# Kernel optimization log

Hardware: AMD Instinct MI355X
Metric: run time of the kernel (lower is better)

The kernel has to match this reference:

```python
import jax, jax.numpy as jnp
import numpy as np

B, L, K, D = 1024, 8, 16, 64
_KSCALE = 1.0 / np.sqrt(K * D)  # keep channel roughly norm-preserving over layers


def setup_inputs() -> dict:
    key = jax.random.key(0)
    k1, k2, k3, k4 = jax.random.split(key, 4)
    state_re = jax.random.normal(k1, (B, D, D), dtype=jnp.float32)
    state_im = jax.random.normal(k2, (B, D, D), dtype=jnp.float32)
    kraus_re = jax.random.normal(k3, (L, K, D, D), dtype=jnp.float32) * _KSCALE
    kraus_im = jax.random.normal(k4, (L, K, D, D), dtype=jnp.float32) * _KSCALE
    return {"state_re": state_re, "state_im": state_im,
            "kraus_re": kraus_re, "kraus_im": kraus_im}


def reference(state_re, state_im, kraus_re, kraus_im):
    # rho: [B, d, d] complex density matrices; kraus: [L, K, d, d]
    rho = (state_re + 1j * state_im).astype(jnp.complex64)
    kraus = (kraus_re + 1j * kraus_im).astype(jnp.complex64)

    def layer_step(rho, Kl):
        # Kl: [K, d, d]. output_state = sum_k  K_k @ rho @ K_k^dagger
        tmp = jnp.einsum('kij,bjl->kbil', Kl, rho)            # K_k @ rho
        rho_new = jnp.einsum('kbil,kml->bim', tmp, Kl.conj())  # (...) @ K_k^dagger, summed over k
        return rho_new, None

    rho, _ = jax.lax.scan(layer_step, rho, kraus)
    # return real/imag stacked as float32: [2, B, d, d]
    return jnp.stack([rho.real, rho.imag])
```

## Files before the change

kernel.cpp:

```cpp
#include <hip/hip_runtime.h>
#include <hip/hip_fp16.h>

#define D 64
#define NKR 16
#define NB 1024
#define NL 8

typedef __attribute__((ext_vector_type(8))) _Float16 half8;
typedef __attribute__((ext_vector_type(16))) float f32x16;
typedef __attribute__((ext_vector_type(4))) int i32x4;

static __device__ __forceinline__ half8 neg8(half8 x) {
    i32x4 u = __builtin_bit_cast(i32x4, x);
    u = u ^ (int)0x80008000;
    return __builtin_bit_cast(half8, u);
}

static __device__ __forceinline__ unsigned pkrtz(float a, float b) {
    auto h = __builtin_amdgcn_cvt_pkrtz(a, b);
    return __builtin_bit_cast(unsigned, h);
}

static __device__ __forceinline__ void plswap(unsigned &a, unsigned &b) {
    asm volatile("v_permlane32_swap_b32 %0, %1" : "+v"(a), "+v"(b));
}

union Pack4 { _Float16 h[4]; uint2 u; };
union H8 { unsigned u[4]; uint2 v[2]; half8 h; };

#define MFMA __builtin_amdgcn_mfma_f32_32x32x16_f16


__global__ void kconv_kernel(const float* __restrict__ re, const float* __restrict__ im,
                             _Float16* __restrict__ out) {
    int plane = blockIdx.y;
    int idx = blockIdx.x * blockDim.x + threadIdx.x;
    const float* src = plane ? im : re;
    float4 v = ((const float4*)src)[idx];
    int e = idx * 4;
    int lk = e >> 12;
    int rem = e & 4095;
    int row = rem >> 6, col = rem & 63;
    int ihalf = row >> 5, r31 = row & 31;
    int ks = col >> 4, hl2 = (col >> 3) & 1, c = col & 7;
    Pack4 p;
    p.h[0] = (_Float16)v.x; p.h[1] = (_Float16)v.y;
    p.h[2] = (_Float16)v.z; p.h[3] = (_Float16)v.w;
    size_t off = (size_t)(lk * 2 + plane) * 4096 + ihalf * 2048
               + (2 * ks + hl2) * 256 + r31 * 8 + c;
    *(uint2*)(out + off) = p.u;
}

__global__ void sconv_kernel(const float* __restrict__ re, const float* __restrict__ im,
                             _Float16* __restrict__ out) {
    __shared__ float tile[64][65];
    int b = blockIdx.x;
    int t = threadIdx.x;
    for (int plane = 0; plane < 2; ++plane) {
        const float* src = (plane ? im : re) + (size_t)b * 4096;
        __syncthreads();
        #pragma unroll
        for (int i = 0; i < 16; ++i) {
            int e = t + 256 * i;
            tile[e >> 6][e & 63] = src[e];
        }
        __syncthreads();
        _Float16* o = out + ((size_t)b * 2 + plane) * 4096;
        #pragma unroll
        for (int i = 0; i < 16; ++i) {
            int oi = t + 256 * i;
            int lh = oi >> 11, slot = (oi >> 8) & 7, r = (oi >> 3) & 31, c = oi & 7;
            int col = 16 * (slot >> 1) + 8 * (slot & 1) + c;
            int row = 32 * lh + r;
            o[oi] = (_Float16)tile[col][row];
        }
    }
}

static __device__ __forceinline__ void exchange(const f32x16 &dd, half8 &f0, half8 &f1) {
    unsigned A0 = pkrtz(dd[0],  dd[1]),  B0 = pkrtz(dd[2],  dd[3]);
    unsigned A1 = pkrtz(dd[4],  dd[5]),  B1 = pkrtz(dd[6],  dd[7]);
    unsigned A2 = pkrtz(dd[8],  dd[9]),  B2 = pkrtz(dd[10], dd[11]);
    unsigned A3 = pkrtz(dd[12], dd[13]), B3 = pkrtz(dd[14], dd[15]);
    plswap(A0, A1);
    plswap(B0, B1);
    plswap(A2, A3);
    plswap(B2, B3);
    H8 h0; h0.u[0] = A0; h0.u[1] = B0; h0.u[2] = A1; h0.u[3] = B1; f0 = h0.h;
    H8 h1; h1.u[0] = A2; h1.u[1] = B2; h1.u[2] = A3; h1.u[3] = B3; f1 = h1.h;
}

template<int IT>
static __device__ __forceinline__ void kstep(
    const _Float16* __restrict__ kb,
    const half8 (&a1re)[2][4], const half8 (&a1im)[2][4],
    f32x16 (&accRe)[2], f32x16 (&accIm)[2],
    int lane)
{
    const _Float16* bo = kb + IT * 2048;
    const _Float16* bx = kb + (1 - IT) * 2048;

    half8 bre[4], bim[4];
    #pragma unroll
    for (int ks = 0; ks < 4; ++ks) {
        bre[ks] = *(const half8*)(bo + ks * 512 + lane * 8);
        bim[ks] = *(const half8*)(bo + 4096 + ks * 512 + lane * 8);
    }

    #pragma unroll
    for (int lh = 0; lh < 2; ++lh) {
        f32x16 ddre, ddim;
        #pragma unroll
        for (int i = 0; i < 16; ++i) { ddre[i] = 0.f; ddim[i] = 0.f; }
        __builtin_amdgcn_s_setprio(1);
        #pragma unroll
        for (int ks = 0; ks < 4; ++ks) {
            half8 bn = neg8(bim[ks]);
            ddre = MFMA(a1re[lh][ks], bre[ks], ddre, 0, 0, 0);
            ddre = MFMA(a1im[lh][ks], bn,      ddre, 0, 0, 0);
            ddim = MFMA(a1re[lh][ks], bim[ks], ddim, 0, 0, 0);
            ddim = MFMA(a1im[lh][ks], bre[ks], ddim, 0, 0, 0);
        }
        __builtin_amdgcn_s_setprio(0);

        half8 br2[2], bi2[2];
        #pragma unroll
        for (int c = 0; c < 2; ++c) {
            const int ks = 2 * lh + c;
            br2[c] = *(const half8*)(bx + ks * 512 + lane * 8);
            bi2[c] = *(const half8*)(bx + 4096 + ks * 512 + lane * 8);
        }

        half8 fre0, fre1, fim0, fim1;
        exchange(ddre, fre0, fre1);
        exchange(ddim, fim0, fim1);

        #pragma unroll
        for (int c = 0; c < 2; ++c) {
            const int ks = 2 * lh + c;
            half8 afre = c ? fre1 : fre0;
            half8 afim = c ? fim1 : fim0;
            half8 an  = neg8(afre);
            __builtin_amdgcn_s_setprio(1);
            accRe[IT]     = MFMA(afre, bre[ks], accRe[IT], 0, 0, 0);
            accRe[IT]     = MFMA(afim, bim[ks], accRe[IT], 0, 0, 0);
            accIm[IT]     = MFMA(afim, bre[ks], accIm[IT], 0, 0, 0);
            accIm[IT]     = MFMA(an,   bim[ks], accIm[IT], 0, 0, 0);
            accRe[1 - IT] = MFMA(afre, br2[c],  accRe[1 - IT], 0, 0, 0);
            accRe[1 - IT] = MFMA(afim, bi2[c],  accRe[1 - IT], 0, 0, 0);
            accIm[1 - IT] = MFMA(afim, br2[c],  accIm[1 - IT], 0, 0, 0);
            accIm[1 - IT] = MFMA(an,   bi2[c],  accIm[1 - IT], 0, 0, 0);
            __builtin_amdgcn_s_setprio(0);
        }
    }
}

template<int IT>
static __device__ __forceinline__ void run_layer(
    const _Float16* __restrict__ kraus,
    const half8 (&a1re)[2][4], const half8 (&a1im)[2][4],
    f32x16 (&accRe)[2], f32x16 (&accIm)[2],
    int lane)
{
    #pragma unroll 1
    for (int k = 0; k < NKR; ++k)
        kstep<IT>(kraus + (size_t)k * 8192, a1re, a1im, accRe, accIm, lane);
}

__global__ __launch_bounds__(64, 2) void layer_kernel(
    const _Float16* __restrict__ rho_in,
    _Float16* __restrict__ rho_out,
    float* __restrict__ final_out,
    const _Float16* __restrict__ kraus,
    int last)
{
    const int b    = blockIdx.x;
    const int IT   = blockIdx.y;
    const int lane = threadIdx.x;
    const int l31  = lane & 31;
    const int hl   = lane >> 5;

    half8 a1re[2][4], a1im[2][4];
    {
        const _Float16* rb = rho_in + (size_t)b * 2 * D * D;
        #pragma unroll
        for (int lh = 0; lh < 2; ++lh)
            #pragma unroll
            for (int ks = 0; ks < 4; ++ks) {
                a1re[lh][ks] = *(const half8*)(rb + lh * 2048 + ks * 512 + lane * 8);
                a1im[lh][ks] = *(const half8*)(rb + 4096 + lh * 2048 + ks * 512 + lane * 8);
            }
    }

    f32x16 accRe[2], accIm[2];
    #pragma unroll
    for (int mt = 0; mt < 2; ++mt)
        #pragma unroll
        for (int i = 0; i < 16; ++i) { accRe[mt][i] = 0.f; accIm[mt][i] = 0.f; }

    if (IT == 0) run_layer<0>(kraus, a1re, a1im, accRe, accIm, lane);
    else         run_layer<1>(kraus, a1re, a1im, accRe, accIm, lane);

    if (!last) {
        _Float16* ob = rho_out + (size_t)b * 2 * D * D;
        #pragma unroll
        for (int mt = 0; mt < 2; ++mt) {
            #pragma unroll
            for (int g = 0; g < 4; ++g) {
                Pack4 pr, pi;
                #pragma unroll
                for (int j = 0; j < 4; ++j) {
                    pr.h[j] = (_Float16)accRe[mt][4 * g + j];
                    pi.h[j] = (_Float16)accIm[mt][4 * g + j];
                }
                const int off = mt * 2048 + (4 * IT + g) * 256 + l31 * 8 + 4 * hl;
                *(uint2*)(ob + off)        = pr.u;
                *(uint2*)(ob + 4096 + off) = pi.u;
            }
        }
    } else {
        float* o0 = final_out + (size_t)b * 4096;
        float* o1 = final_out + (size_t)(NB + b) * 4096;
        #pragma unroll
        for (int mt = 0; mt < 2; ++mt) {
            const int m = 32 * mt + l31;
            #pragma unroll
            for (int g = 0; g < 4; ++g) {
                #pragma unroll
                for (int j = 0; j < 4; ++j) {
                    const int i = 32 * IT + 8 * g + 4 * hl + j;
                    o0[i * D + m] = accRe[mt][4 * g + j];
                    o1[i * D + m] = accIm[mt][4 * g + j];
                }
            }
        }
    }
}

extern "C" void kernel_launch(void* const* d_in, const int* in_sizes, int n_in,
                              void* d_out, int out_size, void* d_ws, size_t ws_size,
                              hipStream_t stream) {
    const float* state_re = (const float*)d_in[0];
    const float* state_im = (const float*)d_in[1];
    const float* kraus_re = (const float*)d_in[2];
    const float* kraus_im = (const float*)d_in[3];

    _Float16* kraus_h = (_Float16*)d_ws;
    _Float16* bufA = (_Float16*)d_out;
    _Float16* bufB = (_Float16*)((char*)d_out + (size_t)NB * 2 * D * D * sizeof(_Float16));
    float* fout = (float*)d_out;

    kconv_kernel<<<dim3(512, 2), 256, 0, stream>>>(kraus_re, kraus_im, kraus_h);
    sconv_kernel<<<NB, 256, 0, stream>>>(state_re, state_im, bufA);

    for (int l = 0; l < NL; ++l) {
        const _Float16* in = (l & 1) ? bufB : bufA;
        _Float16* out      = (l & 1) ? bufA : bufB;
        layer_kernel<<<dim3(NB, 2), 64, 0, stream>>>(in, out, fout,
                                                     kraus_h + (size_t)l * NKR * 2 * D * D,
                                                     (l == NL - 1) ? 1 : 0);
    }
}
```

Baseline: 544.7 us.

## Stream rho fragments from global per Kraus step instead of holding them in registers

Rho operand fragments are no longer preloaded into registers once. Each Kraus step now re-reads them from global memory with one-step-ahead prefetching, and the two row-halves are interleaved so the first GEMM runs four independent accumulation chains. The second-stage B fragments are loaded all at once and the MFMA order is interleaved across accumulators. The aim is to cut register pressure and raise MFMA-level parallelism, at the cost of reloading rho 16 times per block, which relies on L1/L2 hits.

```diff
diff --git a/kernel.cpp b/kernel.cpp
--- a/kernel.cpp
+++ b/kernel.cpp
@@ -93,7 +93,7 @@
 template<int IT>
 static __device__ __forceinline__ void kstep(
     const _Float16* __restrict__ kb,
-    const half8 (&a1re)[2][4], const half8 (&a1im)[2][4],
+    const _Float16* __restrict__ rb,
     f32x16 (&accRe)[2], f32x16 (&accIm)[2],
     int lane)
 {
@@ -107,64 +107,77 @@
         bim[ks] = *(const half8*)(bo + 4096 + ks * 512 + lane * 8);
     }
 
-    #pragma unroll
-    for (int lh = 0; lh < 2; ++lh) {
-        f32x16 ddre, ddim;
-        #pragma unroll
-        for (int i = 0; i < 16; ++i) { ddre[i] = 0.f; ddim[i] = 0.f; }
-        __builtin_amdgcn_s_setprio(1);
-        #pragma unroll
-        for (int ks = 0; ks < 4; ++ks) {
-            half8 bn = neg8(bim[ks]);
-            ddre = MFMA(a1re[lh][ks], bre[ks], ddre, 0, 0, 0);
-            ddre = MFMA(a1im[lh][ks], bn,      ddre, 0, 0, 0);
-            ddim = MFMA(a1re[lh][ks], bim[ks], ddim, 0, 0, 0);
-            ddim = MFMA(a1im[lh][ks], bre[ks], ddim, 0, 0, 0);
-        }
-        __builtin_amdgcn_s_setprio(0);
-
-        half8 br2[2], bi2[2];
-        #pragma unroll
-        for (int c = 0; c < 2; ++c) {
-            const int ks = 2 * lh + c;
-            br2[c] = *(const half8*)(bx + ks * 512 + lane * 8);
-            bi2[c] = *(const half8*)(bx + 4096 + ks * 512 + lane * 8);
-        }
-
-        half8 fre0, fre1, fim0, fim1;
-        exchange(ddre, fre0, fre1);
-        exchange(ddim, fim0, fim1);
-
-        #pragma unroll
-        for (int c = 0; c < 2; ++c) {
-            const int ks = 2 * lh + c;
-            half8 afre = c ? fre1 : fre0;
-            half8 afim = c ? fim1 : fim0;
-            half8 an  = neg8(afre);
-            __builtin_amdgcn_s_setprio(1);
-            accRe[IT]     = MFMA(afre, bre[ks], accRe[IT], 0, 0, 0);
-            accRe[IT]     = MFMA(afim, bim[ks], accRe[IT], 0, 0, 0);
-            accIm[IT]     = MFMA(afim, bre[ks], accIm[IT], 0, 0, 0);
-            accIm[IT]     = MFMA(an,   bim[ks], accIm[IT], 0, 0, 0);
-            accRe[1 - IT] = MFMA(afre, br2[c],  accRe[1 - IT], 0, 0, 0);
-            accRe[1 - IT] = MFMA(afim, bi2[c],  accRe[1 - IT], 0, 0, 0);
-            accIm[1 - IT] = MFMA(afim, br2[c],  accIm[1 - IT], 0, 0, 0);
-            accIm[1 - IT] = MFMA(an,   bi2[c],  accIm[1 - IT], 0, 0, 0);
-            __builtin_amdgcn_s_setprio(0);
-        }
-    }
+    half8 ar0 = *(const half8*)(rb + lane * 8);
+    half8 ai0 = *(const half8*)(rb + 4096 + lane * 8);
+    half8 ar1 = *(const half8*)(rb + 2048 + lane * 8);
+    half8 ai1 = *(const half8*)(rb + 6144 + lane * 8);
+
+    f32x16 dre0, dim0, dre1, dim1;
+    #pragma unroll
+    for (int i = 0; i < 16; ++i) { dre0[i] = 0.f; dim0[i] = 0.f; dre1[i] = 0.f; dim1[i] = 0.f; }
+
+    __builtin_amdgcn_s_setprio(1);
+    #pragma unroll
+    for (int ks = 0; ks < 4; ++ks) {
+        half8 xr0, xi0, xr1, xi1;
+        if (ks < 3) {
+            xr0 = *(const half8*)(rb + (ks + 1) * 512 + lane * 8);
+            xi0 = *(const half8*)(rb + 4096 + (ks + 1) * 512 + lane * 8);
+            xr1 = *(const half8*)(rb + 2048 + (ks + 1) * 512 + lane * 8);
+            xi1 = *(const half8*)(rb + 6144 + (ks + 1) * 512 + lane * 8);
+        }
+        half8 bn = neg8(bim[ks]);
+        dre0 = MFMA(ar0, bre[ks], dre0, 0, 0, 0);
+        dre1 = MFMA(ar1, bre[ks], dre1, 0, 0, 0);
+        dim0 = MFMA(ar0, bim[ks], dim0, 0, 0, 0);
+        dim1 = MFMA(ar1, bim[ks], dim1, 0, 0, 0);
+        dre0 = MFMA(ai0, bn, dre0, 0, 0, 0);
+        dre1 = MFMA(ai1, bn, dre1, 0, 0, 0);
+        dim0 = MFMA(ai0, bre[ks], dim0, 0, 0, 0);
+        dim1 = MFMA(ai1, bre[ks], dim1, 0, 0, 0);
+        if (ks < 3) { ar0 = xr0; ai0 = xi0; ar1 = xr1; ai1 = xi1; }
+    }
+    __builtin_amdgcn_s_setprio(0);
+
+    half8 br2[4], bi2[4];
+    #pragma unroll
+    for (int ks = 0; ks < 4; ++ks) {
+        br2[ks] = *(const half8*)(bx + ks * 512 + lane * 8);
+        bi2[ks] = *(const half8*)(bx + 4096 + ks * 512 + lane * 8);
+    }
+
+    half8 afr[4], afi[4];
+    exchange(dre0, afr[0], afr[1]);
+    exchange(dre1, afr[2], afr[3]);
+    exchange(dim0, afi[0], afi[1]);
+    exchange(dim1, afi[2], afi[3]);
+
+    __builtin_amdgcn_s_setprio(1);
+    #pragma unroll
+    for (int ks = 0; ks < 4; ++ks) {
+        half8 an = neg8(afr[ks]);
+        accRe[IT]     = MFMA(afr[ks], bre[ks], accRe[IT],     0, 0, 0);
+        accIm[IT]     = MFMA(afi[ks], bre[ks], accIm[IT],     0, 0, 0);
+        accRe[1 - IT] = MFMA(afr[ks], br2[ks], accRe[1 - IT], 0, 0, 0);
+        accIm[1 - IT] = MFMA(afi[ks], br2[ks], accIm[1 - IT], 0, 0, 0);
+        accRe[IT]     = MFMA(afi[ks], bim[ks], accRe[IT],     0, 0, 0);
+        accIm[IT]     = MFMA(an,      bim[ks], accIm[IT],     0, 0, 0);
+        accRe[1 - IT] = MFMA(afi[ks], bi2[ks], accRe[1 - IT], 0, 0, 0);
+        accIm[1 - IT] = MFMA(an,      bi2[ks], accIm[1 - IT], 0, 0, 0);
+    }
+    __builtin_amdgcn_s_setprio(0);
 }
 
 template<int IT>
 static __device__ __forceinline__ void run_layer(
     const _Float16* __restrict__ kraus,
-    const half8 (&a1re)[2][4], const half8 (&a1im)[2][4],
+    const _Float16* __restrict__ rb,
     f32x16 (&accRe)[2], f32x16 (&accIm)[2],
     int lane)
 {
     #pragma unroll 1
     for (int k = 0; k < NKR; ++k)
-        kstep<IT>(kraus + (size_t)k * 8192, a1re, a1im, accRe, accIm, lane);
+        kstep<IT>(kraus + (size_t)k * 8192, rb, accRe, accIm, lane);
 }
 
 __global__ __launch_bounds__(64, 2) void layer_kernel(
@@ -180,17 +193,7 @@
     const int l31  = lane & 31;
     const int hl   = lane >> 5;
 
-    half8 a1re[2][4], a1im[2][4];
-    {
-        const _Float16* rb = rho_in + (size_t)b * 2 * D * D;
-        #pragma unroll
-        for (int lh = 0; lh < 2; ++lh)
-            #pragma unroll
-            for (int ks = 0; ks < 4; ++ks) {
-                a1re[lh][ks] = *(const half8*)(rb + lh * 2048 + ks * 512 + lane * 8);
-                a1im[lh][ks] = *(const half8*)(rb + 4096 + lh * 2048 + ks * 512 + lane * 8);
-            }
-    }
+    const _Float16* rb = rho_in + (size_t)b * 2 * D * D;
 
     f32x16 accRe[2], accIm[2];
     #pragma unroll
@@ -198,8 +201,8 @@
         #pragma unroll
         for (int i = 0; i < 16; ++i) { accRe[mt][i] = 0.f; accIm[mt][i] = 0.f; }
 
-    if (IT == 0) run_layer<0>(kraus, a1re, a1im, accRe, accIm, lane);
-    else         run_layer<1>(kraus, a1re, a1im, accRe, accIm, lane);
+    if (IT == 0) run_layer<0>(kraus, rb, accRe, accIm, lane);
+    else         run_layer<1>(kraus, rb, accRe, accIm, lane);
 
     if (!last) {
         _Float16* ob = rho_out + (size_t)b * 2 * D * D;
```

Measured after the change: 589.0 us. +8.1%, slower.

## Fuse all eight layers into one persistent kernel with LDS-resident state

Applied to the files above, without the earlier changes.

Replaces eight per-layer launches with a single kernel in which each block owns one density matrix. Two waves split the row tiles, and the intermediate fp16 state is ping-ponged through shared memory with a barrier after each layer. The initial state is loaded with direct global-to-LDS loads. This removes launch overhead and the global round trips of the intermediate state. In exchange, each block holds 32KB of LDS, which may limit occupancy, and the per-layer barrier serialises the two waves.

```diff
diff --git a/kernel.cpp b/kernel.cpp
--- a/kernel.cpp
+++ b/kernel.cpp
@@ -27,6 +27,10 @@
 
 union Pack4 { _Float16 h[4]; uint2 u; };
 union H8 { unsigned u[4]; uint2 v[2]; half8 h; };
+
+#define GLDS16(gp, lp) \
+    __builtin_amdgcn_global_load_lds((const __attribute__((address_space(1))) void*)(gp), \
+                                     (__attribute__((address_space(3))) void*)(lp), 16, 0, 0)
 
 #define MFMA __builtin_amdgcn_mfma_f32_32x32x16_f16
 
@@ -155,85 +159,93 @@
     }
 }
 
-template<int IT>
-static __device__ __forceinline__ void run_layer(
-    const _Float16* __restrict__ kraus,
-    const half8 (&a1re)[2][4], const half8 (&a1im)[2][4],
-    f32x16 (&accRe)[2], f32x16 (&accIm)[2],
-    int lane)
+__global__ __launch_bounds__(128, 2) void mega_kernel(
+    const _Float16* __restrict__ rho_in,
+    float* __restrict__ final_out,
+    const _Float16* __restrict__ kraus)
 {
-    #pragma unroll 1
-    for (int k = 0; k < NKR; ++k)
-        kstep<IT>(kraus + (size_t)k * 8192, a1re, a1im, accRe, accIm, lane);
-}
-
-__global__ __launch_bounds__(64, 2) void layer_kernel(
-    const _Float16* __restrict__ rho_in,
-    _Float16* __restrict__ rho_out,
-    float* __restrict__ final_out,
-    const _Float16* __restrict__ kraus,
-    int last)
-{
+    __shared__ __align__(16) _Float16 Rlds[2][2 * D * D];
+
     const int b    = blockIdx.x;
-    const int IT   = blockIdx.y;
-    const int lane = threadIdx.x;
+    const int t    = threadIdx.x;
+    const int IT   = t >> 6;
+    const int lane = t & 63;
     const int l31  = lane & 31;
     const int hl   = lane >> 5;
 
-    half8 a1re[2][4], a1im[2][4];
     {
-        const _Float16* rb = rho_in + (size_t)b * 2 * D * D;
+        const char* rb = (const char*)(rho_in + (size_t)b * 2 * D * D);
+        const int off = IT * 8192;
+        #pragma unroll
+        for (int r = 0; r < 8; ++r)
+            GLDS16(rb + off + r * 1024 + lane * 16, (char*)&Rlds[0][0] + off + r * 1024);
+    }
+    __syncthreads();
+
+    #pragma unroll 1
+    for (int l = 0; l < NL; ++l) {
+        const _Float16* rl = &Rlds[l & 1][0];
+        half8 a1re[2][4], a1im[2][4];
         #pragma unroll
         for (int lh = 0; lh < 2; ++lh)
             #pragma unroll
             for (int ks = 0; ks < 4; ++ks) {
-                a1re[lh][ks] = *(const half8*)(rb + lh * 2048 + ks * 512 + lane * 8);
-                a1im[lh][ks] = *(const half8*)(rb + 4096 + lh * 2048 + ks * 512 + lane * 8);
+                a1re[lh][ks] = *(const half8*)(rl + lh * 2048 + ks * 512 + lane * 8);
+                a1im[lh][ks] = *(const half8*)(rl + 4096 + lh * 2048 + ks * 512 + lane * 8);
             }
-    }
-
-    f32x16 accRe[2], accIm[2];
-    #pragma unroll
-    for (int mt = 0; mt < 2; ++mt)
-        #pragma unroll
-        for (int i = 0; i < 16; ++i) { accRe[mt][i] = 0.f; accIm[mt][i] = 0.f; }
-
-    if (IT == 0) run_layer<0>(kraus, a1re, a1im, accRe, accIm, lane);
-    else         run_layer<1>(kraus, a1re, a1im, accRe, accIm, lane);
-
-    if (!last) {
-        _Float16* ob = rho_out + (size_t)b * 2 * D * D;
-        #pragma unroll
-        for (int mt = 0; mt < 2; ++mt) {
-            #pragma unroll
-            for (int g = 0; g < 4; ++g) {
-                Pack4 pr, pi;
+
+        f32x16 accRe[2], accIm[2];
+        #pragma unroll
+        for (int mt = 0; mt < 2; ++mt)
+            #pragma unroll
+            for (int i = 0; i < 16; ++i) { accRe[mt][i] = 0.f; accIm[mt][i] = 0.f; }
+
+        const _Float16* kl = kraus + (size_t)l * NKR * 2 * D * D;
+        if (IT == 0) {
+            #pragma unroll 1
+            for (int k = 0; k < NKR; ++k)
+                kstep<0>(kl + (size_t)k * 8192, a1re, a1im, accRe, accIm, lane);
+        } else {
+            #pragma unroll 1
+            for (int k = 0; k < NKR; ++k)
+                kstep<1>(kl + (size_t)k * 8192, a1re, a1im, accRe, accIm, lane);
+        }
+
+        if (l < NL - 1) {
+            _Float16* ob = &Rlds[(l + 1) & 1][0];
+            #pragma unroll
+            for (int mt = 0; mt < 2; ++mt) {
                 #pragma unroll
-                for (int j = 0; j < 4; ++j) {
-                    pr.h[j] = (_Float16)accRe[mt][4 * g + j];
-                    pi.h[j] = (_Float16)accIm[mt][4 * g + j];
-                }
-                const int off = mt * 2048 + (4 * IT + g) * 256 + l31 * 8 + 4 * hl;
-                *(uint2*)(ob + off)        = pr.u;
-                *(uint2*)(ob + 4096 + off) = pi.u;
-            }
-        }
-    } else {
-        float* o0 = final_out + (size_t)b * 4096;
-        float* o1 = final_out + (size_t)(NB + b) * 4096;
-        #pragma unroll
-        for (int mt = 0; mt < 2; ++mt) {
-            const int m = 32 * mt + l31;
-            #pragma unroll
-            for (int g = 0; g < 4; ++g) {
-                #pragma unroll
-                for (int j = 0; j < 4; ++j) {
-                    const int i = 32 * IT + 8 * g + 4 * hl + j;
-                    o0[i * D + m] = accRe[mt][4 * g + j];
-                    o1[i * D + m] = accIm[mt][4 * g + j];
+                for (int g = 0; g < 4; ++g) {
+                    Pack4 pr, pi;
+                    #pragma unroll
+                    for (int j = 0; j < 4; ++j) {
+                        pr.h[j] = (_Float16)accRe[mt][4 * g + j];
+                        pi.h[j] = (_Float16)accIm[mt][4 * g + j];
+                    }
+                    const int off = mt * 2048 + (4 * IT + g) * 256 + l31 * 8 + 4 * hl;
+                    *(uint2*)(ob + off)        = pr.u;
+                    *(uint2*)(ob + 4096 + off) = pi.u;
                 }
             }
-        }
+        } else {
+            float* o0 = final_out + (size_t)b * 4096;
+            float* o1 = final_out + (size_t)(NB + b) * 4096;
+            #pragma unroll
+            for (int mt = 0; mt < 2; ++mt) {
+                const int m = 32 * mt + l31;
+                #pragma unroll
+                for (int g = 0; g < 4; ++g) {
+                    #pragma unroll
+                    for (int j = 0; j < 4; ++j) {
+                        const int i = 32 * IT + 8 * g + 4 * hl + j;
+                        o0[i * D + m] = accRe[mt][4 * g + j];
+                        o1[i * D + m] = accIm[mt][4 * g + j];
+                    }
+                }
+            }
+        }
+        __syncthreads();
     }
 }
 
@@ -247,17 +259,9 @@
 
     _Float16* kraus_h = (_Float16*)d_ws;
     _Float16* bufA = (_Float16*)d_out;
-    _Float16* bufB = (_Float16*)((char*)d_out + (size_t)NB * 2 * D * D * sizeof(_Float16));
     float* fout = (float*)d_out;
 
     kconv_kernel<<<dim3(512, 2), 256, 0, stream>>>(kraus_re, kraus_im, kraus_h);
     sconv_kernel<<<NB, 256, 0, stream>>>(state_re, state_im, bufA);
-
-    for (int l = 0; l < NL; ++l) {
-        const _Float16* in = (l & 1) ? bufB : bufA;
-        _Float16* out      = (l & 1) ? bufA : bufB;
-        layer_kernel<<<dim3(NB, 2), 64, 0, stream>>>(in, out, fout,
-                                                     kraus_h + (size_t)l * NKR * 2 * D * D,
-                                                     (l == NL - 1) ? 1 : 0);
-    }
-}
+    mega_kernel<<<NB, 128, 0, stream>>>(bufA, fout, kraus_h);
+}
```

New measurement: 517.4 us. 1.05x faster.
